# Performance work log

Hardware: AMD Instinct MI355X
Metric: run time of the kernel (lower is better)

## Reference

```python
import jax, jax.numpy as jnp
import numpy as np

EPS = 1e-10
REG = 1e-6  # regularization_weight passed to sparse_image_warp


def _phi(r2):
    # order-2 polyharmonic (thin-plate) kernel: 0.5 * r^2 * log(r^2)
    return 0.5 * r2 * jnp.log(jnp.maximum(r2, EPS))


def _tps_interpolate(train_pts, train_vals, query_pts, reg):
    # train_pts: (B,N,2), train_vals: (B,N,2), query_pts: (B,Q,2)
    b, n, _ = train_pts.shape
    d2 = jnp.sum((train_pts[:, :, None, :] - train_pts[:, None, :, :]) ** 2, -1)
    A = _phi(d2) + reg * jnp.eye(n, dtype=train_pts.dtype)  # (B,N,N)
    ones_n = jnp.ones((b, n, 1), train_pts.dtype)
    Bm = jnp.concatenate([train_pts, ones_n], -1)  # (B,N,3)
    top = jnp.concatenate([A, Bm], -1)
    bot = jnp.concatenate([jnp.swapaxes(Bm, 1, 2), jnp.zeros((b, 3, 3), train_pts.dtype)], -1)
    lhs = jnp.concatenate([top, bot], 1)  # (B,N+3,N+3)
    rhs = jnp.concatenate([train_vals, jnp.zeros((b, 3, train_vals.shape[-1]), train_vals.dtype)], 1)
    sol = jnp.linalg.solve(lhs, rhs)
    w, v = sol[:, :n], sol[:, n:]  # rbf weights (B,N,2), affine (B,3,2)
    q2 = jnp.sum((query_pts[:, :, None, :] - train_pts[:, None, :, :]) ** 2, -1)  # (B,Q,N)
    rbf = jnp.einsum('bqn,bnd->bqd', _phi(q2), w)
    ones_q = jnp.ones((b, query_pts.shape[1], 1), query_pts.dtype)
    lin = jnp.einsum('bqk,bkd->bqd', jnp.concatenate([query_pts, ones_q], -1), v)
    return rbf + lin


def _bilinear_sample(image, qy, qx):
    # image: (B,H,W,C); qy,qx: (B,Q) float query coordinates (TF dense_image_warp clamping)
    B, H, W, C = image.shape
    y0 = jnp.clip(jnp.floor(qy), 0, H - 2).astype(jnp.int32)
    x0 = jnp.clip(jnp.floor(qx), 0, W - 2).astype(jnp.int32)
    ay = jnp.clip(qy - y0.astype(qy.dtype), 0.0, 1.0)[..., None]
    ax = jnp.clip(qx - x0.astype(qx.dtype), 0.0, 1.0)[..., None]
    bi = jnp.arange(B)[:, None]
    g = lambda yi, xi: image[bi, yi, xi]  # gather -> (B,Q,C)
    top = g(y0, x0) * (1 - ax) + g(y0, x0 + 1) * ax
    bot = g(y0 + 1, x0) * (1 - ax) + g(y0 + 1, x0 + 1) * ax
    return top * (1 - ay) + bot * ay


def _sparse_image_warp(image, src, dst, reg):
    # TF semantics: flows at control points = dst - src, interpolated at dst; sample at grid - flow
    B, H, W, C = image.shape
    flows_ctrl = dst - src  # (B,N,2)
    gy, gx = jnp.meshgrid(jnp.arange(H, dtype=image.dtype), jnp.arange(W, dtype=image.dtype), indexing='ij')
    grid = jnp.broadcast_to(jnp.stack([gy, gx], -1).reshape(1, H * W, 2), (B, H * W, 2))
    dense_flow = _tps_interpolate(dst, flows_ctrl, grid, reg)  # (B,HW,2)
    query = grid - dense_flow
    warped = _bilinear_sample(image, query[..., 0], query[..., 1])
    return warped.reshape(B, H, W, C), dense_flow.reshape(B, H, W, 2)


def setup_inputs() -> dict:
    key = jax.random.key(0)
    ks = jax.random.split(key, 8)
    B, C, H, W = 16, 64, 112, 112
    n_ldmark = 16
    F = C * H * W
    x = jax.random.normal(ks[0], (B, C, H, W), jnp.float32)
    images_rendered = jax.random.normal(ks[1], (B, H, W, C), jnp.float32)
    scales = jax.random.uniform(ks[2], (B, 1), jnp.float32)
    W1 = jax.random.normal(ks[3], (128, F), jnp.float32) / np.float32(np.sqrt(F))
    b1 = jnp.zeros((128,), jnp.float32)
    W2 = jax.random.normal(ks[4], (n_ldmark * 2, 128), jnp.float32) / np.float32(np.sqrt(128))
    b2 = jnp.zeros((n_ldmark * 2,), jnp.float32)
    W3 = jax.random.normal(ks[5], (n_ldmark * 2, 128), jnp.float32) / np.float32(np.sqrt(128))
    b3 = jnp.zeros((n_ldmark * 2,), jnp.float32)
    # torch.normal(mean=0, std=50, size=(n_ldmark,2)) + [0.5*H, 0.5*W], fixed for determinism
    landmarks_mean = jax.random.normal(ks[6], (n_ldmark, 2), jnp.float32) * 50.0 \
        + jnp.array([0.5 * H, 0.5 * W], jnp.float32)
    return {"x": x, "images_rendered": images_rendered, "scales": scales,
            "W1": W1, "b1": b1, "W2": W2, "b2": b2, "W3": W3, "b3": b3,
            "landmarks_mean": landmarks_mean}


def reference(x, images_rendered, scales, W1, b1, W2, b2, W3, b3, landmarks_mean):
    B = x.shape[0]
    n_ldmark = landmarks_mean.shape[0]
    feat = x.reshape(B, -1)
    out = feat @ W1.T + b1  # (B,128)
    landmarks_pred = out @ W2.T + b2 + landmarks_mean.reshape(-1)  # (B, 2*n_ldmark)
    landmarks_disp = (out @ W3.T + b3) * scales
    # original uses .detach().clone() on landmark coords -> stop_gradient
    src = jax.lax.stop_gradient(landmarks_pred).reshape(B, n_ldmark, 2)
    dst = jax.lax.stop_gradient(landmarks_pred + landmarks_disp).reshape(B, n_ldmark, 2)
    # torch.norm(..., dim=(1,2)) = per-batch Frobenius norm, then mean
    landmarks_norm = jnp.mean(jnp.sqrt(jnp.sum((src - dst) ** 2, axis=(1, 2))))
    warped, _dense_flow = _sparse_image_warp(images_rendered, src, dst, REG)
    images_transformed = jnp.transpose(warped, (0, 3, 1, 2))  # NHWC -> NCHW
    return images_transformed, landmarks_pred, landmarks_norm
```

## Files before the change

kernel.cpp:

```cpp
#include <hip/hip_runtime.h>
#include <math.h>
#include <stdint.h>

#define F_K 802816
#define KC 1024
#define NB1 784
#define PRED_OFF 12845056
#define NORM_OFF 12845568

#define AS3 __attribute__((address_space(3)))
#define AS1 __attribute__((address_space(1)))

__device__ __forceinline__ void gload16(const float* gsrc, float* ldsbase) {
#if __has_builtin(__builtin_amdgcn_global_load_lds)
  __builtin_amdgcn_global_load_lds((const AS1 uint32_t*)gsrc, (AS3 uint32_t*)ldsbase, 16, 0, 0);
#else
  int lane = threadIdx.x & 63;
  *reinterpret_cast<float4*>(ldsbase + lane * 4) = *reinterpret_cast<const float4*>(gsrc);
#endif
}

__global__ __launch_bounds__(256) void k_gemm1(const float* __restrict__ x,
                                               const float* __restrict__ w1,
                                               float* __restrict__ part) {
  __shared__ __align__(16) float xs[16 * 64];
  __shared__ __align__(16) float ws[128 * 64];
  const int t = threadIdx.x;
  const int wave = t >> 6, lane = t & 63;
  const int nl = t & 15;
  const int bg = (t >> 4) & 3;
  const size_t k0 = (size_t)blockIdx.x * KC;

  const int xf = wave * 64 + lane;
  const float* xsrc = x + (size_t)(xf >> 4) * F_K + k0 + 4 * (xf & 15);
  float* xdst = xs + wave * 256;

  const float* wsrc[8];
#pragma unroll
  for (int cc = 0; cc < 8; ++cc) {
    int f = (wave * 8 + cc) * 64 + lane;
    int n = f >> 4, c = f & 15;
    int sc = c ^ (n & 7);
    wsrc[cc] = w1 + (size_t)n * F_K + k0 + 4 * sc;
  }
  float* wbase = ws + wave * 2048;

  float acc[4][8];
#pragma unroll
  for (int i = 0; i < 4; ++i)
#pragma unroll
    for (int j = 0; j < 8; ++j) acc[i][j] = 0.f;

  for (int kt = 0; kt < KC / 64; ++kt) {
    gload16(xsrc + kt * 64, xdst);
#pragma unroll
    for (int cc = 0; cc < 8; ++cc) gload16(wsrc[cc] + kt * 64, wbase + cc * 256);
    __syncthreads();
#pragma unroll
    for (int q = 0; q < 4; ++q) {
      const int kk4 = 4 * wave + q;
      float4 xv[4];
#pragma unroll
      for (int i = 0; i < 4; ++i)
        xv[i] = *reinterpret_cast<const float4*>(&xs[(4 * bg + i) * 64 + 4 * kk4]);
      const int c = kk4 ^ (nl & 7);
#pragma unroll
      for (int j = 0; j < 8; ++j) {
        float4 wv = *reinterpret_cast<const float4*>(&ws[(16 * j + nl) * 64 + 4 * c]);
#pragma unroll
        for (int i = 0; i < 4; ++i) {
          acc[i][j] += xv[i].x * wv.x;
          acc[i][j] += xv[i].y * wv.y;
          acc[i][j] += xv[i].z * wv.z;
          acc[i][j] += xv[i].w * wv.w;
        }
      }
    }
    __syncthreads();
  }

  float* red = ws;
#pragma unroll
  for (int i = 0; i < 4; ++i)
#pragma unroll
    for (int j = 0; j < 8; ++j)
      red[wave * 2048 + (4 * bg + i) * 128 + 16 * j + nl] = acc[i][j];
  __syncthreads();
  const int o8 = t * 8;
  float4 s0 = {0, 0, 0, 0}, s1 = {0, 0, 0, 0};
#pragma unroll
  for (int w = 0; w < 4; ++w) {
    float4 a = *reinterpret_cast<const float4*>(&red[w * 2048 + o8]);
    float4 b = *reinterpret_cast<const float4*>(&red[w * 2048 + o8 + 4]);
    s0.x += a.x; s0.y += a.y; s0.z += a.z; s0.w += a.w;
    s1.x += b.x; s1.y += b.y; s1.z += b.z; s1.w += b.w;
  }
  float* pp = part + (size_t)blockIdx.x * 2048 + o8;
  *reinterpret_cast<float4*>(pp) = s0;
  *reinterpret_cast<float4*>(pp + 4) = s1;
}

__global__ __launch_bounds__(256) void k_red(const float* __restrict__ part,
                                             float* __restrict__ p2) {
  int pc = blockIdx.x >> 3, ib = blockIdx.x & 7;
  int idx = ib * 256 + threadIdx.x;
  const float* p = part + (size_t)pc * 49 * 2048 + idx;
  float s = 0.f;
  for (int q = 0; q < 49; ++q) s += p[(size_t)q * 2048];
  p2[pc * 2048 + idx] = s;
}

__global__ __launch_bounds__(64) void k_small(const float* __restrict__ p2,
    const float* __restrict__ b1, const float* __restrict__ W2, const float* __restrict__ b2,
    const float* __restrict__ W3, const float* __restrict__ b3,
    const float* __restrict__ lmean, const float* __restrict__ scales,
    float* __restrict__ dout_pred, float* __restrict__ coef, float* __restrict__ norms) {
  const int b = blockIdx.x, lane = threadIdx.x;
  __shared__ float o[128], dflat[32], fl[32], A[19][22], farr[19], sol[19][2];

  for (int h = 0; h < 2; ++h) {
    int n = lane + 64 * h;
    float s = b1[n];
    for (int pc = 0; pc < 16; ++pc) s += p2[pc * 2048 + b * 128 + n];
    o[n] = s;
  }
  __syncthreads();

  const int j = lane & 31;
  const float* Wm = (lane < 32) ? (W2 + j * 128) : (W3 + j * 128);
  float acc = 0.f;
#pragma unroll 4
  for (int n = 0; n < 128; ++n) acc += o[n] * Wm[n];
  float other = __shfl(acc, j + 32);
  float sc = scales[b];
  float dspv = 0.f;
  if (lane < 32) {
    float predv = acc + b2[j] + lmean[j];
    dspv = (other + b3[j]) * sc;
    dout_pred[b * 32 + j] = predv;
    dflat[j] = predv + dspv;
    fl[j] = dspv;
  }
  float s2 = (lane < 32) ? dspv * dspv : 0.f;
  for (int off = 32; off; off >>= 1) s2 += __shfl_xor(s2, off);
  if (lane == 0) norms[b] = sqrtf(s2);
  __syncthreads();

  for (int cell = lane; cell < 19 * 21; cell += 64) {
    int r = cell / 21, c = cell - (cell / 21) * 21;
    float v;
    if (r < 16) {
      if (c < 16) {
        float dy = dflat[2*r] - dflat[2*c], dx = dflat[2*r+1] - dflat[2*c+1];
        float d2 = dy * dy + dx * dx;
        v = 0.5f * d2 * logf(fmaxf(d2, 1e-10f));
        if (r == c) v += 1e-6f;
      } else if (c == 16) v = dflat[2*r];
      else if (c == 17) v = dflat[2*r+1];
      else if (c == 18) v = 1.0f;
      else if (c == 19) v = fl[2*r];
      else               v = fl[2*r+1];
    } else {
      int rr = r - 16;
      if (c < 16) v = (rr == 0) ? dflat[2*c] : (rr == 1) ? dflat[2*c+1] : 1.0f;
      else        v = 0.0f;
    }
    A[r][c] = v;
  }
  __syncthreads();

  for (int k = 0; k < 19; ++k) {
    float av = (lane >= k && lane < 19) ? fabsf(A[lane][k]) : -1.0f;
    int idx = lane;
    for (int off = 32; off; off >>= 1) {
      float v2 = __shfl_xor(av, off);
      int  i2 = __shfl_xor(idx, off);
      if (v2 > av) { av = v2; idx = i2; }
    }
    idx = __shfl(idx, 0);
    if (idx != k && lane < 21) {
      float tmp = A[k][lane]; A[k][lane] = A[idx][lane]; A[idx][lane] = tmp;
    }
    __syncthreads();
    float invp = 1.0f / A[k][k];
    if (lane < 19) farr[lane] = (lane > k) ? A[lane][k] * invp : 0.0f;
    __syncthreads();
    int nr = 18 - k, nc = 20 - k;
    for (int cell = lane; cell < nr * nc; cell += 64) {
      int i = k + 1 + cell / nc, jj = k + 1 + cell % nc;
      A[i][jj] -= farr[i] * A[k][jj];
    }
    __syncthreads();
  }
  for (int k = 18; k >= 0; --k) {
    if (lane < 2) sol[k][lane] = A[k][19 + lane] / A[k][k];
    __syncthreads();
    if (lane < 2 * k) {
      int i = lane >> 1, c = lane & 1;
      A[i][19 + c] -= A[i][k] * sol[k][c];
    }
    __syncthreads();
  }
  float* cf = coef + b * 80;
  if (lane < 32) { cf[lane] = sol[lane >> 1][lane & 1]; cf[38 + lane] = dflat[lane]; }
  else if (lane < 38) cf[lane] = sol[16 + ((lane - 32) >> 1)][(lane - 32) & 1];
}

__global__ __launch_bounds__(256) void k_warp(const float* __restrict__ img,
                                              const float* __restrict__ coef,
                                              const float* __restrict__ norms,
                                              float* __restrict__ out) {
  const int bid = blockIdx.x;
  const int b = bid / 112, y = bid - (bid / 112) * 112;
  const int t = threadIdx.x;
  __shared__ float qy[112], qx[112];
  __shared__ float cw[32], cv[6], cd[32];
  __shared__ float tile[64][113];

  if (bid == 0 && t == 0) {
    float s = 0.f;
    for (int i = 0; i < 16; ++i) s += norms[i];
    out[NORM_OFF] = s * (1.0f / 16.0f);
  }
  const float* cf = coef + b * 80;
  if (t < 70) {
    float v = cf[t];
    if (t < 32) cw[t] = v;
    else if (t < 38) cv[t - 32] = v;
    else cd[t - 38] = v;
  }
  __syncthreads();

  if (t < 112) {
    float fy = (float)y, fx = (float)t;
    float s0 = cv[0] * fy + cv[2] * fx + cv[4];
    float s1 = cv[1] * fy + cv[3] * fx + cv[5];
#pragma unroll
    for (int i = 0; i < 16; ++i) {
      float dy = fy - cd[2 * i], dx = fx - cd[2 * i + 1];
      float d2 = dy * dy + dx * dx;
      float ph = 0.5f * d2 * logf(fmaxf(d2, 1e-10f));
      s0 += ph * cw[2 * i];
      s1 += ph * cw[2 * i + 1];
    }
    qy[t] = fy - s0;
    qx[t] = fx - s1;
  }
  __syncthreads();

  const int wave = t >> 6, lane = t & 63;
#pragma unroll 4
  for (int p = 0; p < 28; ++p) {
    int xx = wave * 28 + p;
    float fy = qy[xx], fx = qx[xx];
    float y0f = fminf(fmaxf(floorf(fy), 0.f), 110.f);
    float x0f = fminf(fmaxf(floorf(fx), 0.f), 110.f);
    float ay = fminf(fmaxf(fy - y0f, 0.f), 1.f);
    float ax = fminf(fmaxf(fx - x0f, 0.f), 1.f);
    int y0 = (int)y0f, x0 = (int)x0f;
    const float* p00 = img + (((size_t)(b * 112 + y0) * 112 + x0) * 64) + lane;
    float v00 = p00[0], v01 = p00[64];
    float v10 = p00[112 * 64], v11 = p00[112 * 64 + 64];
    float top = v00 * (1.f - ax) + v01 * ax;
    float bot = v10 * (1.f - ax) + v11 * ax;
    tile[lane][xx] = top * (1.f - ay) + bot * ay;
  }
  __syncthreads();

  float* ob = out + (size_t)b * 64 * 12544 + y * 112;
  for (int i = 0; i < 28; ++i) {
    int idx = i * 256 + t;
    int c = idx / 112, xx = idx - c * 112;
    ob[(size_t)c * 12544 + xx] = tile[c][xx];
  }
}

extern "C" void kernel_launch(void* const* d_in, const int* in_sizes, int n_in,
                              void* d_out, int out_size, void* d_ws, size_t ws_size,
                              hipStream_t stream) {
  const float* x      = (const float*)d_in[0];
  const float* img    = (const float*)d_in[1];
  const float* scales = (const float*)d_in[2];
  const float* W1     = (const float*)d_in[3];
  const float* b1     = (const float*)d_in[4];
  const float* W2     = (const float*)d_in[5];
  const float* b2     = (const float*)d_in[6];
  const float* W3     = (const float*)d_in[7];
  const float* b3     = (const float*)d_in[8];
  const float* lmean  = (const float*)d_in[9];
  float* out = (float*)d_out;
  float* ws  = (float*)d_ws;

  float* P1   = ws;
  float* P2   = P1 + (size_t)NB1 * 2048;
  float* COEF = P2 + 16 * 2048;
  float* NORM = COEF + 16 * 80;

  k_gemm1<<<NB1, 256, 0, stream>>>(x, W1, P1);
  k_red  <<<128, 256, 0, stream>>>(P1, P2);
  k_small<<<16, 64, 0, stream>>>(P2, b1, W2, b2, W3, b3, lmean, scales,
                                 out + PRED_OFF, COEF, NORM);
  k_warp <<<16 * 112, 256, 0, stream>>>(img, COEF, NORM, out);
}
```

Before: 184.1 us.

## Double-buffer GEMM1 LDS loads and fuse partial reduction into small solver kernel

The GEMM1 kernel now uses two LDS buffers and issues the next tile's global-to-LDS loads before computing on the current one, with explicit vmcnt waits and raw barriers, so load latency overlaps compute. The separate k_red kernel is removed and k_small reduces all 784 partials directly with 256 threads, saving a launch. The single-wave solver section drops its __syncthreads calls and relies on wave-level lockstep for LDS ordering. Doubling LDS may lower occupancy, and the partial reduction now runs on only 16 blocks.

```diff
diff --git a/kernel.cpp b/kernel.cpp
--- a/kernel.cpp
+++ b/kernel.cpp
@@ -12,19 +12,14 @@
 #define AS1 __attribute__((address_space(1)))
 
 __device__ __forceinline__ void gload16(const float* gsrc, float* ldsbase) {
-#if __has_builtin(__builtin_amdgcn_global_load_lds)
   __builtin_amdgcn_global_load_lds((const AS1 uint32_t*)gsrc, (AS3 uint32_t*)ldsbase, 16, 0, 0);
-#else
-  int lane = threadIdx.x & 63;
-  *reinterpret_cast<float4*>(ldsbase + lane * 4) = *reinterpret_cast<const float4*>(gsrc);
-#endif
 }
 
 __global__ __launch_bounds__(256) void k_gemm1(const float* __restrict__ x,
                                                const float* __restrict__ w1,
                                                float* __restrict__ part) {
-  __shared__ __align__(16) float xs[16 * 64];
-  __shared__ __align__(16) float ws[128 * 64];
+  __shared__ __align__(16) float xs[2][16 * 64];
+  __shared__ __align__(16) float ws[2][128 * 64];
   const int t = threadIdx.x;
   const int wave = t >> 6, lane = t & 63;
   const int nl = t & 15;
@@ -33,17 +28,14 @@
 
   const int xf = wave * 64 + lane;
   const float* xsrc = x + (size_t)(xf >> 4) * F_K + k0 + 4 * (xf & 15);
-  float* xdst = xs + wave * 256;
 
   const float* wsrc[8];
 #pragma unroll
   for (int cc = 0; cc < 8; ++cc) {
     int f = (wave * 8 + cc) * 64 + lane;
     int n = f >> 4, c = f & 15;
-    int sc = c ^ (n & 7);
-    wsrc[cc] = w1 + (size_t)n * F_K + k0 + 4 * sc;
-  }
-  float* wbase = ws + wave * 2048;
+    wsrc[cc] = w1 + (size_t)n * F_K + k0 + 4 * (c ^ (n & 7));
+  }
 
   float acc[4][8];
 #pragma unroll
@@ -51,22 +43,34 @@
 #pragma unroll
     for (int j = 0; j < 8; ++j) acc[i][j] = 0.f;
 
+  gload16(xsrc, &xs[0][wave * 256]);
+#pragma unroll
+  for (int cc = 0; cc < 8; ++cc) gload16(wsrc[cc], &ws[0][wave * 2048 + cc * 256]);
+
   for (int kt = 0; kt < KC / 64; ++kt) {
-    gload16(xsrc + kt * 64, xdst);
-#pragma unroll
-    for (int cc = 0; cc < 8; ++cc) gload16(wsrc[cc] + kt * 64, wbase + cc * 256);
-    __syncthreads();
+    const int cur = kt & 1;
+    if (kt < KC / 64 - 1) {
+      const int nxt = cur ^ 1;
+      gload16(xsrc + (kt + 1) * 64, &xs[nxt][wave * 256]);
+#pragma unroll
+      for (int cc = 0; cc < 8; ++cc)
+        gload16(wsrc[cc] + (kt + 1) * 64, &ws[nxt][wave * 2048 + cc * 256]);
+      asm volatile("s_waitcnt vmcnt(9)" ::: "memory");
+    } else {
+      asm volatile("s_waitcnt vmcnt(0)" ::: "memory");
+    }
+    __builtin_amdgcn_s_barrier();
 #pragma unroll
     for (int q = 0; q < 4; ++q) {
       const int kk4 = 4 * wave + q;
       float4 xv[4];
 #pragma unroll
       for (int i = 0; i < 4; ++i)
-        xv[i] = *reinterpret_cast<const float4*>(&xs[(4 * bg + i) * 64 + 4 * kk4]);
+        xv[i] = *reinterpret_cast<const float4*>(&xs[cur][(4 * bg + i) * 64 + 4 * kk4]);
       const int c = kk4 ^ (nl & 7);
 #pragma unroll
       for (int j = 0; j < 8; ++j) {
-        float4 wv = *reinterpret_cast<const float4*>(&ws[(16 * j + nl) * 64 + 4 * c]);
+        float4 wv = *reinterpret_cast<const float4*>(&ws[cur][(16 * j + nl) * 64 + 4 * c]);
 #pragma unroll
         for (int i = 0; i < 4; ++i) {
           acc[i][j] += xv[i].x * wv.x;
@@ -76,10 +80,10 @@
         }
       }
     }
-    __syncthreads();
-  }
-
-  float* red = ws;
+    __builtin_amdgcn_s_barrier();
+  }
+
+  float* red = &ws[0][0];
 #pragma unroll
   for (int i = 0; i < 4; ++i)
 #pragma unroll
@@ -100,31 +104,29 @@
   *reinterpret_cast<float4*>(pp + 4) = s1;
 }
 
-__global__ __launch_bounds__(256) void k_red(const float* __restrict__ part,
-                                             float* __restrict__ p2) {
-  int pc = blockIdx.x >> 3, ib = blockIdx.x & 7;
-  int idx = ib * 256 + threadIdx.x;
-  const float* p = part + (size_t)pc * 49 * 2048 + idx;
-  float s = 0.f;
-  for (int q = 0; q < 49; ++q) s += p[(size_t)q * 2048];
-  p2[pc * 2048 + idx] = s;
-}
-
-__global__ __launch_bounds__(64) void k_small(const float* __restrict__ p2,
+__global__ __launch_bounds__(256) void k_small(const float* __restrict__ part,
     const float* __restrict__ b1, const float* __restrict__ W2, const float* __restrict__ b2,
     const float* __restrict__ W3, const float* __restrict__ b3,
     const float* __restrict__ lmean, const float* __restrict__ scales,
     float* __restrict__ dout_pred, float* __restrict__ coef, float* __restrict__ norms) {
-  const int b = blockIdx.x, lane = threadIdx.x;
+  const int b = blockIdx.x, t = threadIdx.x;
+  __shared__ float o2[2][128];
   __shared__ float o[128], dflat[32], fl[32], A[19][22], farr[19], sol[19][2];
 
-  for (int h = 0; h < 2; ++h) {
-    int n = lane + 64 * h;
-    float s = b1[n];
-    for (int pc = 0; pc < 16; ++pc) s += p2[pc * 2048 + b * 128 + n];
-    o[n] = s;
-  }
-  __syncthreads();
+  {
+    const int n = t & 127, h = t >> 7;
+    const float* p = part + (size_t)h * 2048 + b * 128 + n;
+    float s = 0.f;
+#pragma unroll 8
+    for (int q = 0; q < 392; ++q) s += p[(size_t)q * 4096];
+    o2[h][n] = s;
+  }
+  __syncthreads();
+  if (t >= 64) return;
+
+  const int lane = t;
+  o[lane]      = o2[0][lane]      + o2[1][lane]      + b1[lane];
+  o[lane + 64] = o2[0][lane + 64] + o2[1][lane + 64] + b1[lane + 64];
 
   const int j = lane & 31;
   const float* Wm = (lane < 32) ? (W2 + j * 128) : (W3 + j * 128);
@@ -144,7 +146,6 @@
   float s2 = (lane < 32) ? dspv * dspv : 0.f;
   for (int off = 32; off; off >>= 1) s2 += __shfl_xor(s2, off);
   if (lane == 0) norms[b] = sqrtf(s2);
-  __syncthreads();
 
   for (int cell = lane; cell < 19 * 21; cell += 64) {
     int r = cell / 21, c = cell - (cell / 21) * 21;
@@ -167,7 +168,6 @@
     }
     A[r][c] = v;
   }
-  __syncthreads();
 
   for (int k = 0; k < 19; ++k) {
     float av = (lane >= k && lane < 19) ? fabsf(A[lane][k]) : -1.0f;
@@ -181,25 +181,20 @@
     if (idx != k && lane < 21) {
       float tmp = A[k][lane]; A[k][lane] = A[idx][lane]; A[idx][lane] = tmp;
     }
-    __syncthreads();
     float invp = 1.0f / A[k][k];
     if (lane < 19) farr[lane] = (lane > k) ? A[lane][k] * invp : 0.0f;
-    __syncthreads();
     int nr = 18 - k, nc = 20 - k;
     for (int cell = lane; cell < nr * nc; cell += 64) {
       int i = k + 1 + cell / nc, jj = k + 1 + cell % nc;
       A[i][jj] -= farr[i] * A[k][jj];
     }
-    __syncthreads();
   }
   for (int k = 18; k >= 0; --k) {
     if (lane < 2) sol[k][lane] = A[k][19 + lane] / A[k][k];
-    __syncthreads();
     if (lane < 2 * k) {
       int i = lane >> 1, c = lane & 1;
       A[i][19 + c] -= A[i][k] * sol[k][c];
     }
-    __syncthreads();
   }
   float* cf = coef + b * 80;
   if (lane < 32) { cf[lane] = sol[lane >> 1][lane & 1]; cf[38 + lane] = dflat[lane]; }
@@ -292,13 +287,11 @@
   float* ws  = (float*)d_ws;
 
   float* P1   = ws;
-  float* P2   = P1 + (size_t)NB1 * 2048;
-  float* COEF = P2 + 16 * 2048;
+  float* COEF = P1 + (size_t)NB1 * 2048;
   float* NORM = COEF + 16 * 80;
 
   k_gemm1<<<NB1, 256, 0, stream>>>(x, W1, P1);
-  k_red  <<<128, 256, 0, stream>>>(P1, P2);
-  k_small<<<16, 64, 0, stream>>>(P2, b1, W2, b2, W3, b3, lmean, scales,
-                                 out + PRED_OFF, COEF, NORM);
+  k_small<<<16, 256, 0, stream>>>(P1, b1, W2, b2, W3, b3, lmean, scales,
+                                  out + PRED_OFF, COEF, NORM);
   k_warp <<<16 * 112, 256, 0, stream>>>(img, COEF, NORM, out);
 }
```

After: 212.5 us. 1.15x slower.

## Make gemm1 LDS tiles wave-private and drop per-iteration block barriers

Applied to the files above, without the earlier changes.

Reorganizes the LDS staging so each wave loads and consumes only its own 16-element k-slice of x and W1. This replaces the two block-wide __syncthreads per k-step with per-wave s_waitcnt vmcnt/lgkmcnt waits. A new rotation swizzle replaces the XOR swizzle to avoid LDS bank conflicts in the new layout. The change relies on global_load_lds completion semantics via vmcnt and removes the non-builtin fallback path.

```diff
diff --git a/kernel.cpp b/kernel.cpp
--- a/kernel.cpp
+++ b/kernel.cpp
@@ -12,37 +12,35 @@
 #define AS1 __attribute__((address_space(1)))
 
 __device__ __forceinline__ void gload16(const float* gsrc, float* ldsbase) {
-#if __has_builtin(__builtin_amdgcn_global_load_lds)
   __builtin_amdgcn_global_load_lds((const AS1 uint32_t*)gsrc, (AS3 uint32_t*)ldsbase, 16, 0, 0);
-#else
-  int lane = threadIdx.x & 63;
-  *reinterpret_cast<float4*>(ldsbase + lane * 4) = *reinterpret_cast<const float4*>(gsrc);
-#endif
 }
 
 __global__ __launch_bounds__(256) void k_gemm1(const float* __restrict__ x,
                                                const float* __restrict__ w1,
                                                float* __restrict__ part) {
-  __shared__ __align__(16) float xs[16 * 64];
-  __shared__ __align__(16) float ws[128 * 64];
+  __shared__ __align__(16) float xs[256 * 4];
+  __shared__ __align__(16) float ws[2048 * 4];
   const int t = threadIdx.x;
   const int wave = t >> 6, lane = t & 63;
   const int nl = t & 15;
   const int bg = (t >> 4) & 3;
   const size_t k0 = (size_t)blockIdx.x * KC;
 
-  const int xf = wave * 64 + lane;
-  const float* xsrc = x + (size_t)(xf >> 4) * F_K + k0 + 4 * (xf & 15);
-  float* xdst = xs + wave * 256;
-
   const float* wsrc[8];
 #pragma unroll
   for (int cc = 0; cc < 8; ++cc) {
-    int f = (wave * 8 + cc) * 64 + lane;
-    int n = f >> 4, c = f & 15;
-    int sc = c ^ (n & 7);
-    wsrc[cc] = w1 + (size_t)n * F_K + k0 + 4 * sc;
-  }
+    int flat = cc * 64 + lane;
+    int n = flat >> 2, tau = flat & 3;
+    int q = (tau - (n >> 1)) & 3;
+    wsrc[cc] = w1 + (size_t)n * F_K + k0 + 16 * wave + 4 * q;
+  }
+  const float* xsrc;
+  {
+    int b = lane >> 2, tau = lane & 3;
+    int q = (tau - (b >> 1)) & 3;
+    xsrc = x + (size_t)b * F_K + k0 + 16 * wave + 4 * q;
+  }
+  float* xbase = xs + wave * 256;
   float* wbase = ws + wave * 2048;
 
   float acc[4][8];
@@ -52,21 +50,25 @@
     for (int j = 0; j < 8; ++j) acc[i][j] = 0.f;
 
   for (int kt = 0; kt < KC / 64; ++kt) {
-    gload16(xsrc + kt * 64, xdst);
+    asm volatile("s_waitcnt lgkmcnt(0)" ::: "memory");
+    gload16(xsrc + kt * 64, xbase);
 #pragma unroll
     for (int cc = 0; cc < 8; ++cc) gload16(wsrc[cc] + kt * 64, wbase + cc * 256);
-    __syncthreads();
+    asm volatile("s_waitcnt vmcnt(0)" ::: "memory");
+    __builtin_amdgcn_sched_barrier(0);
 #pragma unroll
     for (int q = 0; q < 4; ++q) {
-      const int kk4 = 4 * wave + q;
       float4 xv[4];
 #pragma unroll
-      for (int i = 0; i < 4; ++i)
-        xv[i] = *reinterpret_cast<const float4*>(&xs[(4 * bg + i) * 64 + 4 * kk4]);
-      const int c = kk4 ^ (nl & 7);
+      for (int i = 0; i < 4; ++i) {
+        int b = 4 * bg + i;
+        int tx = (q + (b >> 1)) & 3;
+        xv[i] = *reinterpret_cast<const float4*>(&xbase[b * 16 + 4 * tx]);
+      }
+      const int tw = (q + (nl >> 1)) & 3;
 #pragma unroll
       for (int j = 0; j < 8; ++j) {
-        float4 wv = *reinterpret_cast<const float4*>(&ws[(16 * j + nl) * 64 + 4 * c]);
+        float4 wv = *reinterpret_cast<const float4*>(&wbase[(16 * j + nl) * 16 + 4 * tw]);
 #pragma unroll
         for (int i = 0; i < 4; ++i) {
           acc[i][j] += xv[i].x * wv.x;
@@ -76,9 +78,9 @@
         }
       }
     }
-    __syncthreads();
-  }
-
+  }
+
+  __syncthreads();
   float* red = ws;
 #pragma unroll
   for (int i = 0; i < 4; ++i)
```

New measurement: 177.7 us. -3.5%, faster.
